# Kernel tuning notes

Measured on AMD Instinct MI355X. Metric: run time of the kernel, lower is better.

## Reference

```python
import jax, jax.numpy as jnp
import numpy as np

N_VOCAB, N_REL, D_EMB, D_HID, N_MOTIF = 200000, 50, 128, 128, 85
N_NODES, N_EDGES, N_CENTER, N_NONMOL = 100000, 600000, 512, 20000


def _l2norm(x):
    # torch F.normalize(p=2, dim=1) with eps=1e-12
    n = jnp.linalg.norm(x, axis=1, keepdims=True)
    return x / jnp.maximum(n, 1e-12)


def _gine(x, src, dst, edge_attr, W, b):
    # GINEConv(eps=0): Linear(x + segment_sum(relu(x[src] + edge_attr), dst))
    m = jax.nn.relu(x[src] + edge_attr)            # [E, H]
    agg = jax.ops.segment_sum(m, dst, num_segments=x.shape[0])  # [N, H]
    return (x + agg) @ W + b


def setup_inputs() -> dict:
    key = jax.random.key(0)
    ks = jax.random.split(key, 20)
    s = lambda k, shape, fan: jax.random.normal(k, shape, jnp.float32) * (1.0 / np.sqrt(fan))
    inp = {
        'node_ids': jax.random.randint(ks[0], (N_NODES,), 0, N_VOCAB),
        'rel_ids': jax.random.randint(ks[1], (N_EDGES,), 0, N_REL),
        'center_mol_idx': jax.random.randint(ks[2], (N_CENTER,), 0, N_NODES),
        'non_molecule_node_ids': jax.random.randint(ks[3], (N_NONMOL,), 0, N_NODES),
        'edge_index': jax.random.randint(ks[4], (2, N_EDGES), 0, N_NODES),
        # learned params (weights stored [in, out], i.e. torch W.T)
        'node_emb_table': jax.random.normal(ks[5], (N_VOCAB, D_EMB), jnp.float32),
        'rel_emb_table': jax.random.normal(ks[6], (N_REL, D_EMB), jnp.float32),
        'lin_W': s(ks[7], (D_EMB, D_HID), D_EMB), 'lin_b': jnp.zeros((D_HID,), jnp.float32),
        'W1': s(ks[8], (D_HID, D_HID), D_HID), 'b1': jnp.zeros((D_HID,), jnp.float32),
        'W2': s(ks[9], (D_HID, D_HID), D_HID), 'b2': jnp.zeros((D_HID,), jnp.float32),
        'edge_W': s(ks[10], (2 * D_HID, N_REL), 2 * D_HID), 'edge_b': jnp.zeros((N_REL,), jnp.float32),
        'motif_W': s(ks[11], (D_HID, N_MOTIF), D_HID), 'motif_b': jnp.zeros((N_MOTIF,), jnp.float32),
        'nodec_W': s(ks[12], (D_HID, 15), D_HID), 'nodec_b': jnp.zeros((15,), jnp.float32),
        'bin_W': s(ks[13], (D_HID, 1), D_HID), 'bin_b': jnp.zeros((1,), jnp.float32),
    }
    return inp


def reference(node_ids, rel_ids, center_mol_idx, non_molecule_node_ids, edge_index,
              node_emb_table, rel_emb_table, lin_W, lin_b, W1, b1, W2, b2,
              edge_W, edge_b, motif_W, motif_b, nodec_W, nodec_b, bin_W, bin_b):
    x = _l2norm(node_emb_table[node_ids])          # [N, D]
    e = _l2norm(rel_emb_table[rel_ids])            # [E, D]
    x = jax.nn.relu(x @ lin_W + lin_b)             # [N, H]
    e = jax.nn.relu(e @ lin_W + lin_b)             # [E, H]
    src, dst = edge_index[0], edge_index[1]
    x = jax.nn.relu(_gine(x, src, dst, e, W1, b1))
    x = _gine(x, src, dst, e, W2, b2)              # [N, H]
    edge_pred_input = jnp.concatenate([x[src], x[dst]], axis=1)   # [E, 2H]
    edge_class = edge_pred_input @ edge_W + edge_b                 # [E, num_rels]
    motif_pred = x[center_mol_idx] @ motif_W + motif_b             # [B, num_motifs]
    node_class = x[non_molecule_node_ids] @ nodec_W + nodec_b      # [M, 15]
    binary_pred = x @ bin_W + bin_b                                # [N, 1]
    return (edge_class, motif_pred, node_class, binary_pred)
```

## Files before the change

kernel.cpp:

```cpp
#include <hip/hip_runtime.h>
#include <hip/hip_bf16.h>
#include <math.h>

typedef __hip_bfloat16 bf16;
typedef __attribute__((ext_vector_type(8))) short short8;
typedef __attribute__((ext_vector_type(4))) float float4v;

#define N_NODES_C 100000
#define N_EDGES_C 600000
#define N_CENTER_C 512
#define N_NONMOL_C 20000
#define N_REL_C 50
#define D_C 128
#define N_MOTIF_C 85

#define EO_EDGE  0L
#define EO_MOTIF 30000000L
#define EO_NODEC 30043520L
#define EO_BIN   30343520L

#define AGG_OFF  0L
#define ET_OFF   51200000L
#define WT0_OFF  51225600L
#define WT1_OFF  51258368L
#define WT2_OFF  51291136L
#define BPQ_OFF  51323904L
#define LB_OFF   51352576L
#define B1_OFF   51353088L
#define B2_OFF   51353600L
#define OFFS_OFF 51354112L
#define BSUM_OFF 51755680L
#define SSRC_OFF 51757248L
#define SREL_OFF 54157248L

__device__ __forceinline__ float b2f(bf16 v) { return __bfloat162float(v); }
__device__ __forceinline__ float bits2f(unsigned short s) {
    unsigned u = ((unsigned)s) << 16; float f; __builtin_memcpy(&f, &u, 4); return f;
}
__device__ __forceinline__ unsigned short f2bits(float f) {
    bf16 h = __float2bfloat16(f); unsigned short s; __builtin_memcpy(&s, &h, 2); return s;
}
__device__ __forceinline__ float ldf(const void* p, size_t i, int isbf) {
    return isbf ? __bfloat162float(((const bf16*)p)[i]) : ((const float*)p)[i];
}
__device__ __forceinline__ void stout(void* p, size_t i, int isbf, float v) {
    if (isbf) ((bf16*)p)[i] = __float2bfloat16(v);
    else      ((float*)p)[i] = v;
}

__global__ void probe_kernel(const void* __restrict__ table, int* __restrict__ flag) {
    __shared__ int bad[256];
    int t = threadIdx.x;
    const bf16* p = (const bf16*)table;
    int cnt = 0;
    for (int i = 0; i < 64; i++) {
        float v = __bfloat162float(p[t * 64 + i]);
        if (!isfinite(v) || fabsf(v) > 1000.0f) cnt++;
    }
    bad[t] = cnt;
    __syncthreads();
    for (int s = 128; s > 0; s >>= 1) {
        if (t < s) bad[t] += bad[t + s];
        __syncthreads();
    }
    if (t == 0) *flag = (bad[0] == 0) ? 1 : 0;
}

__global__ void prepack_kernel(const int* __restrict__ flag,
                               const void* __restrict__ linW, const void* __restrict__ w1,
                               const void* __restrict__ w2, const void* __restrict__ edgeW,
                               const void* __restrict__ linb, const void* __restrict__ bb1,
                               const void* __restrict__ bb2,
                               unsigned short* __restrict__ WT0, unsigned short* __restrict__ WT1,
                               unsigned short* __restrict__ WT2, unsigned short* __restrict__ BPQ,
                               float* __restrict__ LB, float* __restrict__ B1p, float* __restrict__ B2p) {
    int isbf = *flag;
    int g = blockIdx.x * 256 + threadIdx.x;
    if (g < 3 * 16384) {
        int w = g / 16384, i = g % 16384;
        int n = i >> 7, k = i & 127;
        const void* src = (w == 0) ? linW : (w == 1) ? w1 : w2;
        unsigned short* dst = (w == 0) ? WT0 : (w == 1) ? WT1 : WT2;
        dst[i] = f2bits(ldf(src, (size_t)k * 128 + n, isbf));
    } else if (g < 3 * 16384 + 112 * 128) {
        int i = g - 3 * 16384;
        int j = i >> 7, k = i & 127;
        float v = 0.0f;
        if (j < 50)       v = ldf(edgeW, (size_t)k * 50 + j, isbf);
        else if (j < 100) v = ldf(edgeW, (size_t)(128 + k) * 50 + (j - 50), isbf);
        BPQ[i] = f2bits(v);
    } else if (g < 3 * 16384 + 112 * 128 + 3 * 128) {
        int i = g - (3 * 16384 + 112 * 128);
        int w = i >> 7, n = i & 127;
        const void* src = (w == 0) ? linb : (w == 1) ? bb1 : bb2;
        float* dst = (w == 0) ? LB : (w == 1) ? B1p : B2p;
        dst[n] = ldf(src, n, isbf);
    }
}

__global__ void et_kernel(const int* __restrict__ flag,
                          const void* __restrict__ table,
                          const void* __restrict__ W,
                          const void* __restrict__ bias,
                          float* __restrict__ out) {
    int isbf = *flag;
    int row = blockIdx.x;
    int t = threadIdx.x;
    float v = ldf(table, (size_t)row * D_C + t, isbf);
    __shared__ float sv[D_C];
    __shared__ float red[D_C];
    red[t] = v * v;
    __syncthreads();
    for (int s = 64; s > 0; s >>= 1) {
        if (t < s) red[t] += red[t + s];
        __syncthreads();
    }
    float nrm = fmaxf(sqrtf(red[0]), 1e-12f);
    sv[t] = v / nrm;
    __syncthreads();
    float acc = ldf(bias, t, isbf);
    for (int k = 0; k < D_C; k++) acc = fmaf(sv[k], ldf(W, k * D_C + t, isbf), acc);
    out[(size_t)row * D_C + t] = fmaxf(acc, 0.0f);
}

__global__ void normalize_kernel(const int* __restrict__ flag,
                                 const int* __restrict__ ids,
                                 const void* __restrict__ table,
                                 unsigned short* __restrict__ out) {
    int w = (int)((blockIdx.x * (long)blockDim.x + threadIdx.x) >> 6);
    int lane = threadIdx.x & 63;
    if (w >= N_NODES_C) return;
    int isbf = *flag;
    int id = ids[w];
    float v0, v1;
    if (isbf) {
        const unsigned short* p = (const unsigned short*)table + (size_t)id * D_C + lane * 2;
        ushort2 u = *(const ushort2*)p;
        v0 = bits2f(u.x); v1 = bits2f(u.y);
    } else {
        const float* p = (const float*)table + (size_t)id * D_C + lane * 2;
        float2 f = *(const float2*)p;
        v0 = f.x; v1 = f.y;
    }
    float ss = v0 * v0 + v1 * v1;
#pragma unroll
    for (int o = 32; o > 0; o >>= 1) ss += __shfl_down(ss, o, 64);
    ss = __shfl(ss, 0, 64);
    float inv = 1.0f / fmaxf(sqrtf(ss), 1e-12f);
    ushort2 o2;
    o2.x = f2bits(v0 * inv);
    o2.y = f2bits(v1 * inv);
    *(ushort2*)(out + (size_t)w * D_C + lane * 2) = o2;
}

template <int NOUT, bool RELU, bool ADD_AGG, bool HAS_BIAS>
__global__ __launch_bounds__(256, 2) void gemm_kernel(
        const unsigned short* __restrict__ X,
        const float* __restrict__ AGG,
        const unsigned short* __restrict__ BT,
        const float* __restrict__ bias,
        unsigned short* __restrict__ Y,
        int M) {
    constexpr int NT = (NOUT + 15) / 16;
    __shared__ short Als[128 * 128];
    __shared__ short Bls[NT * 16 * 128];
    int t = threadIdx.x;
    int m0 = blockIdx.x * 128;

#pragma unroll
    for (int p = 0; p < 8; p++) {
        int lin = (p * 256 + t) * 8;
        int row = lin >> 7, col = lin & 127;
        int gr = m0 + row; if (gr >= M) gr = M - 1;
        short8 xv = *(const short8*)(X + (size_t)gr * 128 + col);
        if (ADD_AGG) {
            const float* ap = AGG + (size_t)gr * 128 + col;
            float4v a0 = *(const float4v*)ap;
            float4v a1 = *(const float4v*)(ap + 4);
            short8 r;
#pragma unroll
            for (int i = 0; i < 4; i++) r[i] = (short)f2bits(bits2f((unsigned short)xv[i]) + a0[i]);
#pragma unroll
            for (int i = 0; i < 4; i++) r[4 + i] = (short)f2bits(bits2f((unsigned short)xv[4 + i]) + a1[i]);
            xv = r;
        }
        *(short8*)&Als[lin] = xv;
    }
    constexpr int BELEMS = NT * 16 * 128;
#pragma unroll
    for (int p = 0; p * 2048 < BELEMS; p++) {
        int lin = (p * 256 + t) * 8;
        if (lin < BELEMS) *(short8*)&Bls[lin] = *(const short8*)(BT + lin);
    }
    __syncthreads();

    int wave = t >> 6, lane = t & 63;
    int quad = lane >> 4, lr = lane & 15;
    int wr0 = wave * 32;

    short8 afr[2][4];
#pragma unroll
    for (int mt = 0; mt < 2; mt++)
#pragma unroll
        for (int kk = 0; kk < 4; kk++)
            afr[mt][kk] = *(short8*)&Als[(wr0 + mt * 16 + lr) * 128 + kk * 32 + quad * 8];

#pragma unroll
    for (int nt = 0; nt < NT; nt++) {
        short8 bfr[4];
#pragma unroll
        for (int kk = 0; kk < 4; kk++)
            bfr[kk] = *(short8*)&Bls[(nt * 16 + lr) * 128 + kk * 32 + quad * 8];
        int col = nt * 16 + lr;
        float bs = 0.0f;
        if (HAS_BIAS) bs = bias[col];
#pragma unroll
        for (int mt = 0; mt < 2; mt++) {
            float4v acc = {0.0f, 0.0f, 0.0f, 0.0f};
#pragma unroll
            for (int kk = 0; kk < 4; kk++)
                acc = __builtin_amdgcn_mfma_f32_16x16x32_bf16(afr[mt][kk], bfr[kk], acc, 0, 0, 0);
            int rbase = m0 + wr0 + mt * 16 + quad * 4;
#pragma unroll
            for (int r = 0; r < 4; r++) {
                int row = rbase + r;
                float v = acc[r] + bs;
                if (RELU) v = fmaxf(v, 0.0f);
                if (row < M && ((NOUT & 15) == 0 || col < NOUT))
                    Y[(size_t)row * NOUT + col] = f2bits(v);
            }
        }
    }
}

__global__ void hist_kernel(const int* __restrict__ ei, int* __restrict__ cnt) {
    int e = blockIdx.x * 256 + threadIdx.x;
    if (e < N_EDGES_C) atomicAdd(&cnt[ei[N_EDGES_C + e]], 1);
}

__global__ void scan1_kernel(int* __restrict__ cnt, int* __restrict__ bsum) {
    __shared__ int s[256];
    int t = threadIdx.x;
    int idx = blockIdx.x * 256 + t;
    int v = (idx < N_NODES_C) ? cnt[idx] : 0;
    s[t] = v;
    __syncthreads();
    for (int o = 1; o < 256; o <<= 1) {
        int u = (t >= o) ? s[t - o] : 0;
        __syncthreads();
        s[t] += u;
        __syncthreads();
    }
    if (idx < N_NODES_C) cnt[idx] = s[t] - v;
    if (t == 255) bsum[blockIdx.x] = s[255];
}

__global__ void scan2_kernel(int* __restrict__ bsum, int nb) {
    __shared__ int s[512];
    int t = threadIdx.x;
    int v = (t < nb) ? bsum[t] : 0;
    s[t] = v;
    __syncthreads();
    for (int o = 1; o < 512; o <<= 1) {
        int u = (t >= o) ? s[t - o] : 0;
        __syncthreads();
        s[t] += u;
        __syncthreads();
    }
    if (t < nb) bsum[t] = s[t] - v;
}

__global__ void scan3_kernel(int* __restrict__ cnt, const int* __restrict__ bsum) {
    int idx = blockIdx.x * 256 + threadIdx.x;
    if (idx < N_NODES_C) cnt[idx] += bsum[blockIdx.x];
}

__global__ void sort_scatter_kernel(const int* __restrict__ ei, const int* __restrict__ rel,
                                    int* __restrict__ offs,
                                    int* __restrict__ ssrc, int* __restrict__ srel) {
    int e = blockIdx.x * 256 + threadIdx.x;
    if (e >= N_EDGES_C) return;
    int dst = ei[N_EDGES_C + e];
    int pos = atomicAdd(&offs[dst], 1);
    ssrc[pos] = ei[e];
    srel[pos] = rel[e];
}

__global__ __launch_bounds__(256) void gather_agg_kernel(
        const unsigned short* __restrict__ x,
        const int* __restrict__ offs,
        const int* __restrict__ ssrc, const int* __restrict__ srel,
        const float* __restrict__ etab,
        float* __restrict__ agg) {
    int t = threadIdx.x;
    int node = blockIdx.x * 2 + (t >> 7);
    int feat = t & 127;
    if (node >= N_NODES_C) return;
    int start = (node == 0) ? 0 : offs[node - 1];
    int end = offs[node];
    float acc = 0.0f;
    for (int e = start; e < end; e++) {
        int src = ssrc[e];
        int r = srel[e];
        acc += fmaxf(bits2f(x[(size_t)src * D_C + feat]) + etab[r * D_C + feat], 0.0f);
    }
    agg[(size_t)node * D_C + feat] = acc;
}

__global__ void edge_out_kernel(const int* __restrict__ flag,
                                const int* __restrict__ ei,
                                const unsigned short* __restrict__ PQ,
                                const void* __restrict__ eb,
                                void* __restrict__ out) {
    int isbf = *flag;
    long g = (long)blockIdx.x * blockDim.x + threadIdx.x;
    if (g >= (long)N_EDGES_C * N_REL_C) return;
    int e = (int)(g / N_REL_C);
    int j = (int)(g - (long)e * N_REL_C);
    int src = ei[e];
    int dst = ei[N_EDGES_C + e];
    float v = bits2f(PQ[(size_t)src * 100 + j]) + bits2f(PQ[(size_t)dst * 100 + 50 + j]) + ldf(eb, j, isbf);
    stout(out, EO_EDGE + g, isbf, v);
}

__global__ void motif_kernel(const int* __restrict__ flag,
                             const int* __restrict__ cidx,
                             const bf16* __restrict__ x,
                             const void* __restrict__ W,
                             const void* __restrict__ bias,
                             void* __restrict__ out) {
    int isbf = *flag;
    int row = blockIdx.x;
    int t = threadIdx.x;
    __shared__ float sv[D_C];
    int id = cidx[row];
    sv[t] = b2f(x[(size_t)id * D_C + t]);
    __syncthreads();
    if (t < N_MOTIF_C) {
        float acc = ldf(bias, t, isbf);
        for (int k = 0; k < D_C; k++) acc = fmaf(sv[k], ldf(W, k * N_MOTIF_C + t, isbf), acc);
        stout(out, EO_MOTIF + (size_t)row * N_MOTIF_C + t, isbf, acc);
    }
}

__global__ void nodec_kernel(const int* __restrict__ flag,
                             const int* __restrict__ nidx,
                             const bf16* __restrict__ x,
                             const void* __restrict__ W,
                             const void* __restrict__ bias,
                             void* __restrict__ out) {
    int isbf = *flag;
    int g = blockIdx.x * blockDim.x + threadIdx.x;
    if (g >= N_NONMOL_C * 15) return;
    int row = g / 15;
    int j = g - row * 15;
    int id = nidx[row];
    float acc = ldf(bias, j, isbf);
    for (int k = 0; k < D_C; k++) acc = fmaf(b2f(x[(size_t)id * D_C + k]), ldf(W, k * 15 + j, isbf), acc);
    stout(out, EO_NODEC + g, isbf, acc);
}

__global__ void binary_kernel(const int* __restrict__ flag,
                              const bf16* __restrict__ x,
                              const void* __restrict__ W,
                              const void* __restrict__ bias,
                              void* __restrict__ out) {
    int isbf = *flag;
    int g = blockIdx.x * blockDim.x + threadIdx.x;
    int row = g >> 6;
    int lane = threadIdx.x & 63;
    if (row >= N_NODES_C) return;
    float a = b2f(x[(size_t)row * D_C + lane]) * ldf(W, lane, isbf) +
              b2f(x[(size_t)row * D_C + 64 + lane]) * ldf(W, 64 + lane, isbf);
#pragma unroll
    for (int off = 32; off > 0; off >>= 1) a += __shfl_down(a, off, 64);
    if (lane == 0) stout(out, EO_BIN + row, isbf, a + ldf(bias, 0, isbf));
}

extern "C" void kernel_launch(void* const* d_in, const int* in_sizes, int n_in,
                              void* d_out, int out_size, void* d_ws, size_t ws_size,
                              hipStream_t stream) {
    const int* node_ids = (const int*)d_in[0];
    const int* rel_ids  = (const int*)d_in[1];
    const int* center   = (const int*)d_in[2];
    const int* nonmol   = (const int*)d_in[3];
    const int* ei       = (const int*)d_in[4];
    const void* node_emb = d_in[5];
    const void* rel_emb  = d_in[6];
    const void* lin_W = d_in[7];
    const void* lin_b = d_in[8];
    const void* W1 = d_in[9];
    const void* b1 = d_in[10];
    const void* W2 = d_in[11];
    const void* b2 = d_in[12];
    const void* edge_W = d_in[13];
    const void* edge_b = d_in[14];
    const void* motif_W = d_in[15];
    const void* motif_b = d_in[16];
    const void* nodec_W = d_in[17];
    const void* nodec_b = d_in[18];
    const void* bin_W = d_in[19];
    const void* bin_b = d_in[20];

    char* wsb = (char*)d_ws;
    unsigned short* X0 = (unsigned short*)wsb;
    unsigned short* X1 = (unsigned short*)(wsb + (size_t)N_NODES_C * D_C * 2);
    int* FLAG = (int*)(wsb + (size_t)2 * N_NODES_C * D_C * 2);
    unsigned short* PQ = X1;

    char* ob = (char*)d_out;
    float* AGG = (float*)(ob + AGG_OFF);
    float* ET  = (float*)(ob + ET_OFF);
    unsigned short* WT0 = (unsigned short*)(ob + WT0_OFF);
    unsigned short* WT1 = (unsigned short*)(ob + WT1_OFF);
    unsigned short* WT2 = (unsigned short*)(ob + WT2_OFF);
    unsigned short* BPQ = (unsigned short*)(ob + BPQ_OFF);
    float* LB  = (float*)(ob + LB_OFF);
    float* B1p = (float*)(ob + B1_OFF);
    float* B2p = (float*)(ob + B2_OFF);
    int* OFFS = (int*)(ob + OFFS_OFF);
    int* BSUM = (int*)(ob + BSUM_OFF);
    int* SSRC = (int*)(ob + SSRC_OFF);
    int* SREL = (int*)(ob + SREL_OFF);

    const int gemm_blocks = (N_NODES_C + 127) / 128;
    const int nscan = (N_NODES_C + 255) / 256;
    const int eblocks = (N_EDGES_C + 255) / 256;

    probe_kernel<<<1, 256, 0, stream>>>(node_emb, FLAG);
    prepack_kernel<<<250, 256, 0, stream>>>(FLAG, lin_W, W1, W2, edge_W, lin_b, b1, b2,
                                            WT0, WT1, WT2, BPQ, LB, B1p, B2p);
    et_kernel<<<N_REL_C, D_C, 0, stream>>>(FLAG, rel_emb, lin_W, lin_b, ET);

    hipMemsetAsync(OFFS, 0, N_NODES_C * sizeof(int), stream);
    hist_kernel<<<eblocks, 256, 0, stream>>>(ei, OFFS);
    scan1_kernel<<<nscan, 256, 0, stream>>>(OFFS, BSUM);
    scan2_kernel<<<1, 512, 0, stream>>>(BSUM, nscan);
    scan3_kernel<<<nscan, 256, 0, stream>>>(OFFS, BSUM);
    sort_scatter_kernel<<<eblocks, 256, 0, stream>>>(ei, rel_ids, OFFS, SSRC, SREL);

    normalize_kernel<<<(N_NODES_C * 64 + 255) / 256, 256, 0, stream>>>(FLAG, node_ids, node_emb, X0);
    gemm_kernel<128, true, false, true><<<gemm_blocks, 256, 0, stream>>>(X0, nullptr, WT0, LB, X0, N_NODES_C);

    gather_agg_kernel<<<(N_NODES_C + 1) / 2, 256, 0, stream>>>(X0, OFFS, SSRC, SREL, ET, AGG);
    gemm_kernel<128, true, true, true><<<gemm_blocks, 256, 0, stream>>>(X0, AGG, WT1, B1p, X1, N_NODES_C);

    gather_agg_kernel<<<(N_NODES_C + 1) / 2, 256, 0, stream>>>(X1, OFFS, SSRC, SREL, ET, AGG);
    gemm_kernel<128, false, true, true><<<gemm_blocks, 256, 0, stream>>>(X1, AGG, WT2, B2p, X0, N_NODES_C);

    gemm_kernel<100, false, false, false><<<gemm_blocks, 256, 0, stream>>>(X0, nullptr, BPQ, nullptr, PQ, N_NODES_C);

    long ethreads = (long)N_EDGES_C * N_REL_C;
    edge_out_kernel<<<(int)((ethreads + 255) / 256), 256, 0, stream>>>(FLAG, ei, PQ, edge_b, d_out);

    motif_kernel<<<N_CENTER_C, D_C, 0, stream>>>(FLAG, center, (const bf16*)X0, motif_W, motif_b, d_out);
    nodec_kernel<<<(N_NONMOL_C * 15 + 255) / 256, 256, 0, stream>>>(FLAG, nonmol, (const bf16*)X0, nodec_W, nodec_b, d_out);
    binary_kernel<<<(N_NODES_C * 64 + 255) / 256, 256, 0, stream>>>(FLAG, (const bf16*)X0, bin_W, bin_b, d_out);
}
```

Before: 832.6 us.

## Switch GINE aggregation to edge-parallel segmented reduction with boundary atomics

Replaces the node-per-128-threads gather aggregation with a wave-per-32-sorted-edges scheme. Each lane handles two features, and partial sums are written directly for segments that are interior to a wave, or with atomics at the segment boundaries. This balances work across nodes with uneven degree and vectorizes the index loads. The cost is a sorted destination array, a memset of the aggregation buffer before each layer, and some float atomics that make summation order nondeterministic.

```diff
diff --git a/kernel.cpp b/kernel.cpp
--- a/kernel.cpp
+++ b/kernel.cpp
@@ -32,6 +32,9 @@
 #define BSUM_OFF 51755680L
 #define SSRC_OFF 51757248L
 #define SREL_OFF 54157248L
+#define SDST_OFF 56557248L
+
+#define EPW_C 32
 
 __device__ __forceinline__ float b2f(bf16 v) { return __bfloat162float(v); }
 __device__ __forceinline__ float bits2f(unsigned short s) {
@@ -277,34 +280,63 @@
 
 __global__ void sort_scatter_kernel(const int* __restrict__ ei, const int* __restrict__ rel,
                                     int* __restrict__ offs,
-                                    int* __restrict__ ssrc, int* __restrict__ srel) {
+                                    int* __restrict__ ssrc, int* __restrict__ srel,
+                                    int* __restrict__ sdst) {
     int e = blockIdx.x * 256 + threadIdx.x;
     if (e >= N_EDGES_C) return;
     int dst = ei[N_EDGES_C + e];
     int pos = atomicAdd(&offs[dst], 1);
     ssrc[pos] = ei[e];
     srel[pos] = rel[e];
-}
-
-__global__ __launch_bounds__(256) void gather_agg_kernel(
+    sdst[pos] = dst;
+}
+
+__global__ __launch_bounds__(256) void gather_agg2_kernel(
         const unsigned short* __restrict__ x,
-        const int* __restrict__ offs,
         const int* __restrict__ ssrc, const int* __restrict__ srel,
+        const int* __restrict__ sdst,
         const float* __restrict__ etab,
         float* __restrict__ agg) {
-    int t = threadIdx.x;
-    int node = blockIdx.x * 2 + (t >> 7);
-    int feat = t & 127;
-    if (node >= N_NODES_C) return;
-    int start = (node == 0) ? 0 : offs[node - 1];
-    int end = offs[node];
-    float acc = 0.0f;
-    for (int e = start; e < end; e++) {
-        int src = ssrc[e];
-        int r = srel[e];
-        acc += fmaxf(bits2f(x[(size_t)src * D_C + feat]) + etab[r * D_C + feat], 0.0f);
-    }
-    agg[(size_t)node * D_C + feat] = acc;
+    int w = (int)((blockIdx.x * 256u + threadIdx.x) >> 6);
+    int lane = threadIdx.x & 63;
+    int e0 = w * EPW_C;
+    if (e0 >= N_EDGES_C) return;
+
+    float a0 = 0.0f, a1 = 0.0f;
+    int cur = sdst[e0];
+    bool first = true;
+
+    for (int e = e0; e < e0 + EPW_C; e += 4) {
+        int4 sv = *(const int4*)(ssrc + e);
+        int4 rv = *(const int4*)(srel + e);
+        int4 dv = *(const int4*)(sdst + e);
+        ushort2 u0 = *(const ushort2*)(x + (size_t)sv.x * D_C + lane * 2);
+        ushort2 u1 = *(const ushort2*)(x + (size_t)sv.y * D_C + lane * 2);
+        ushort2 u2 = *(const ushort2*)(x + (size_t)sv.z * D_C + lane * 2);
+        ushort2 u3 = *(const ushort2*)(x + (size_t)sv.w * D_C + lane * 2);
+        float2 t0 = *(const float2*)(etab + rv.x * D_C + lane * 2);
+        float2 t1 = *(const float2*)(etab + rv.y * D_C + lane * 2);
+        float2 t2 = *(const float2*)(etab + rv.z * D_C + lane * 2);
+        float2 t3 = *(const float2*)(etab + rv.w * D_C + lane * 2);
+        int d[4] = {dv.x, dv.y, dv.z, dv.w};
+        ushort2 uu[4] = {u0, u1, u2, u3};
+        float2 tt[4] = {t0, t1, t2, t3};
+#pragma unroll
+        for (int j = 0; j < 4; j++) {
+            if (d[j] != cur) {
+                float* p = agg + (size_t)cur * D_C + lane * 2;
+                if (first) { atomicAdd(p, a0); atomicAdd(p + 1, a1); }
+                else       { p[0] = a0; p[1] = a1; }
+                first = false; a0 = 0.0f; a1 = 0.0f; cur = d[j];
+            }
+            a0 += fmaxf(bits2f(uu[j].x) + tt[j].x, 0.0f);
+            a1 += fmaxf(bits2f(uu[j].y) + tt[j].y, 0.0f);
+        }
+    }
+    bool endshere = (e0 + EPW_C >= N_EDGES_C) || (sdst[e0 + EPW_C] != cur);
+    float* p = agg + (size_t)cur * D_C + lane * 2;
+    if (!first && endshere) { p[0] = a0; p[1] = a1; }
+    else { atomicAdd(p, a0); atomicAdd(p + 1, a1); }
 }
 
 __global__ void edge_out_kernel(const int* __restrict__ flag,
@@ -422,10 +454,13 @@
     int* BSUM = (int*)(ob + BSUM_OFF);
     int* SSRC = (int*)(ob + SSRC_OFF);
     int* SREL = (int*)(ob + SREL_OFF);
+    int* SDST = (int*)(ob + SDST_OFF);
 
     const int gemm_blocks = (N_NODES_C + 127) / 128;
     const int nscan = (N_NODES_C + 255) / 256;
     const int eblocks = (N_EDGES_C + 255) / 256;
+    const int g2_waves = N_EDGES_C / EPW_C;
+    const int g2_blocks = (g2_waves + 3) / 4;
 
     probe_kernel<<<1, 256, 0, stream>>>(node_emb, FLAG);
     prepack_kernel<<<250, 256, 0, stream>>>(FLAG, lin_W, W1, W2, edge_W, lin_b, b1, b2,
@@ -437,15 +472,17 @@
     scan1_kernel<<<nscan, 256, 0, stream>>>(OFFS, BSUM);
     scan2_kernel<<<1, 512, 0, stream>>>(BSUM, nscan);
     scan3_kernel<<<nscan, 256, 0, stream>>>(OFFS, BSUM);
-    sort_scatter_kernel<<<eblocks, 256, 0, stream>>>(ei, rel_ids, OFFS, SSRC, SREL);
+    sort_scatter_kernel<<<eblocks, 256, 0, stream>>>(ei, rel_ids, OFFS, SSRC, SREL, SDST);
 
     normalize_kernel<<<(N_NODES_C * 64 + 255) / 256, 256, 0, stream>>>(FLAG, node_ids, node_emb, X0);
     gemm_kernel<128, true, false, true><<<gemm_blocks, 256, 0, stream>>>(X0, nullptr, WT0, LB, X0, N_NODES_C);
 
-    gather_agg_kernel<<<(N_NODES_C + 1) / 2, 256, 0, stream>>>(X0, OFFS, SSRC, SREL, ET, AGG);
+    hipMemsetAsync(AGG, 0, (size_t)N_NODES_C * D_C * sizeof(float), stream);
+    gather_agg2_kernel<<<g2_blocks, 256, 0, stream>>>(X0, SSRC, SREL, SDST, ET, AGG);
     gemm_kernel<128, true, true, true><<<gemm_blocks, 256, 0, stream>>>(X0, AGG, WT1, B1p, X1, N_NODES_C);
 
-    gather_agg_kernel<<<(N_NODES_C + 1) / 2, 256, 0, stream>>>(X1, OFFS, SSRC, SREL, ET, AGG);
+    hipMemsetAsync(AGG, 0, (size_t)N_NODES_C * D_C * sizeof(float), stream);
+    gather_agg2_kernel<<<g2_blocks, 256, 0, stream>>>(X1, SSRC, SREL, SDST, ET, AGG);
     gemm_kernel<128, false, true, true><<<gemm_blocks, 256, 0, stream>>>(X1, AGG, WT2, B2p, X0, N_NODES_C);
 
     gemm_kernel<100, false, false, false><<<gemm_blocks, 256, 0, stream>>>(X0, nullptr, BPQ, nullptr, PQ, N_NODES_C);
```

New measurement: 717.2 us. 13.9% less time.
